# Kernel optimization log

Hardware: AMD Instinct MI355X
Metric: run time of the kernel (lower is better)

## Reference

```python
import jax, jax.numpy as jnp
import numpy as np

V = 256      # vocab_size (hard-coded in source)
H = 2048     # hidden_size
S = 2048     # encoder input length
T = 2048     # decoder target length


def _gru_cell(x, h, w_ih, w_hh, b_ih, b_hh):
    # PyTorch GRU cell math. x, h: [H]; w_ih, w_hh: [3H, H]; b_*: [3H]
    gi = w_ih @ x + b_ih
    gh = w_hh @ h + b_hh
    i_r, i_z, i_n = jnp.split(gi, 3)
    h_r, h_z, h_n = jnp.split(gh, 3)
    r = jax.nn.sigmoid(i_r + h_r)
    z = jax.nn.sigmoid(i_z + h_z)
    n = jnp.tanh(i_n + r * h_n)
    return (1.0 - z) * n + z * h


def setup_inputs() -> dict:
    key = jax.random.key(0)
    ks = jax.random.split(key, 16)
    k = 1.0 / np.sqrt(H)
    u = lambda kk, shape: jax.random.uniform(kk, shape, jnp.float32, -k, k)
    return {
        "inputs": jax.random.randint(ks[0], (S,), 0, V),
        "targets": jax.random.randint(ks[1], (T,), 0, V),
        "emb": jax.random.normal(ks[2], (V, H), jnp.float32),
        "enc_w_ih": u(ks[3], (3 * H, H)),
        "enc_w_hh": u(ks[4], (3 * H, H)),
        "enc_b_ih": u(ks[5], (3 * H,)),
        "enc_b_hh": u(ks[6], (3 * H,)),
        "dec_w_ih": u(ks[7], (3 * H, H)),
        "dec_w_hh": u(ks[8], (3 * H, H)),
        "dec_b_ih": u(ks[9], (3 * H,)),
        "dec_b_hh": u(ks[10], (3 * H,)),
        "fc_w": u(ks[11], (V, H)),
        "fc_b": u(ks[12], (V,)),
    }


def reference(inputs, targets, emb, enc_w_ih, enc_w_hh, enc_b_ih, enc_b_hh,
              dec_w_ih, dec_w_hh, dec_b_ih, dec_b_hh, fc_w, fc_b):
    # Encoder: run GRU over embedded input sequence, keep final state.
    enc_x = emb[inputs]                      # [S, H]
    h0 = jnp.zeros((H,), dtype=emb.dtype)

    def enc_step(h, x):
        return _gru_cell(x, h, enc_w_ih, enc_w_hh, enc_b_ih, enc_b_hh), None

    h_enc, _ = jax.lax.scan(enc_step, h0, enc_x)

    # Decoder token stream: step 0 uses token 0; every later step uses the
    # SAME token targets[1] (faithful to the bug in the original source).
    dec_tokens = jnp.where(jnp.arange(T) == 0, 0, targets[1])  # [T]
    dec_x = emb[dec_tokens]                  # [T, H]

    def dec_step(h, x):
        h_new = _gru_cell(x, h, dec_w_ih, dec_w_hh, dec_b_ih, dec_b_hh)
        return h_new, h_new

    _, dec_hs = jax.lax.scan(dec_step, h_enc, dec_x)  # [T, H]

    # Output projection (batch dim of 1 squeezed away as in the original).
    return dec_hs @ fc_w.T + fc_b            # [T, V]
```

## Files before the change

### kernel.cpp

```cpp
#include <hip/hip_runtime.h>
#include <hip/hip_fp16.h>

#define Hh 2048
#define VV 256
#define SS 2048
#define TT 2048
#define NB 128
#define NT 512

typedef _Float16 h4 __attribute__((ext_vector_type(4)));
typedef _Float16 h2 __attribute__((ext_vector_type(2)));
typedef unsigned int u32x4 __attribute__((ext_vector_type(4)));
typedef unsigned short u16x4 __attribute__((ext_vector_type(4)));

#if defined(__has_builtin)
#if __has_builtin(__builtin_amdgcn_fdot2)
#define FDOT2(a, b, c) __builtin_amdgcn_fdot2((a), (b), (c), false)
#endif
#endif
#ifndef FDOT2
#define FDOT2(a, b, c) \
  fmaf((float)(a).x, (float)(b).x, fmaf((float)(a).y, (float)(b).y, (c)))
#endif

#define SH(v, a, b) __builtin_shufflevector((v), (v), (a), (b))

__global__ __launch_bounds__(256) void gemm_nt(const float* __restrict__ A,
                                               const float* __restrict__ B,
                                               const float* __restrict__ biasM,
                                               const float* __restrict__ biasN,
                                               float* __restrict__ C,
                                               int M, int N, int K) {
  __shared__ __align__(16) float At[32][68];
  __shared__ __align__(16) float Bt[32][68];
  const int t = threadIdx.x;
  const int m0 = blockIdx.x << 6, n0 = blockIdx.y << 6;
  const int r0 = t >> 3, c4 = (t & 7) << 2;
  const int tm = (t >> 4) << 2, tn = (t & 15) << 2;
  float acc[4][4];
#pragma unroll
  for (int i = 0; i < 4; ++i)
#pragma unroll
    for (int j = 0; j < 4; ++j) acc[i][j] = 0.f;

  for (int k0 = 0; k0 < K; k0 += 32) {
    float4 a0 = *(const float4*)&A[(size_t)(m0 + r0) * K + k0 + c4];
    float4 a1 = *(const float4*)&A[(size_t)(m0 + r0 + 32) * K + k0 + c4];
    float4 b0 = *(const float4*)&B[(size_t)(n0 + r0) * K + k0 + c4];
    float4 b1 = *(const float4*)&B[(size_t)(n0 + r0 + 32) * K + k0 + c4];
    __syncthreads();
    At[c4 + 0][r0] = a0.x; At[c4 + 1][r0] = a0.y; At[c4 + 2][r0] = a0.z; At[c4 + 3][r0] = a0.w;
    At[c4 + 0][r0 + 32] = a1.x; At[c4 + 1][r0 + 32] = a1.y; At[c4 + 2][r0 + 32] = a1.z; At[c4 + 3][r0 + 32] = a1.w;
    Bt[c4 + 0][r0] = b0.x; Bt[c4 + 1][r0] = b0.y; Bt[c4 + 2][r0] = b0.z; Bt[c4 + 3][r0] = b0.w;
    Bt[c4 + 0][r0 + 32] = b1.x; Bt[c4 + 1][r0 + 32] = b1.y; Bt[c4 + 2][r0 + 32] = b1.z; Bt[c4 + 3][r0 + 32] = b1.w;
    __syncthreads();
#pragma unroll
    for (int k = 0; k < 32; ++k) {
      float4 av = *(const float4*)&At[k][tm];
      float4 bv = *(const float4*)&Bt[k][tn];
      acc[0][0] = fmaf(av.x, bv.x, acc[0][0]);
      acc[0][1] = fmaf(av.x, bv.y, acc[0][1]);
      acc[0][2] = fmaf(av.x, bv.z, acc[0][2]);
      acc[0][3] = fmaf(av.x, bv.w, acc[0][3]);
      acc[1][0] = fmaf(av.y, bv.x, acc[1][0]);
      acc[1][1] = fmaf(av.y, bv.y, acc[1][1]);
      acc[1][2] = fmaf(av.y, bv.z, acc[1][2]);
      acc[1][3] = fmaf(av.y, bv.w, acc[1][3]);
      acc[2][0] = fmaf(av.z, bv.x, acc[2][0]);
      acc[2][1] = fmaf(av.z, bv.y, acc[2][1]);
      acc[2][2] = fmaf(av.z, bv.z, acc[2][2]);
      acc[2][3] = fmaf(av.z, bv.w, acc[2][3]);
      acc[3][0] = fmaf(av.w, bv.x, acc[3][0]);
      acc[3][1] = fmaf(av.w, bv.y, acc[3][1]);
      acc[3][2] = fmaf(av.w, bv.z, acc[3][2]);
      acc[3][3] = fmaf(av.w, bv.w, acc[3][3]);
    }
  }
#pragma unroll
  for (int i = 0; i < 4; ++i) {
    float bm = biasM ? biasM[m0 + tm + i] : 0.f;
#pragma unroll
    for (int j = 0; j < 4; ++j) {
      float bn = biasN ? biasN[n0 + tn + j] : 0.f;
      C[(size_t)(m0 + tm + i) * N + n0 + tn + j] = acc[i][j] + bm + bn;
    }
  }
}

__global__ __launch_bounds__(NT) void recur_kernel(
    const float* __restrict__ giT_enc, const float* __restrict__ giT_dec,
    const float* __restrict__ enc_w_hh, const float* __restrict__ enc_b_hh,
    const float* __restrict__ dec_w_hh, const float* __restrict__ dec_b_hh,
    const int* __restrict__ inputs, const int* __restrict__ targets,
    unsigned int* __restrict__ hb, float* __restrict__ dec_hs) {
  __shared__ __align__(16) float gi_lds[48 * VV];
  __shared__ __align__(16) _Float16 h16[2][Hh];
  __shared__ __align__(16) unsigned short tok_lds[SS];
  __shared__ float gidec_lds[96];

  const int t = threadIdx.x;
  const int b = blockIdx.x;
  const int bks = b << 4;
  const int w = t >> 6, l = t & 63;
  const int ri = (w << 1) + (l & 1);

  h4 wregA[24], wregB[24];
  float br_, bz_, bn_;
  auto load_wb = [&](const float* W, const float* B) {
#pragma unroll
    for (int g = 0; g < 3; ++g) {
      const float* r0 = W + ((size_t)(g * Hh + bks + (w << 1) + 0)) * Hh + (l << 2);
      const float* r1 = W + ((size_t)(g * Hh + bks + (w << 1) + 1)) * Hh + (l << 2);
#pragma unroll
      for (int q = 0; q < 8; ++q) {
        float4 v0 = *(const float4*)&r0[q * 256];
        float4 v1 = *(const float4*)&r1[q * 256];
        wregA[g * 8 + q] = h4{(_Float16)v0.x, (_Float16)v0.y,
                             (_Float16)v0.z, (_Float16)v0.w};
        wregB[g * 8 + q] = h4{(_Float16)v1.x, (_Float16)v1.y,
                             (_Float16)v1.z, (_Float16)v1.w};
      }
    }
    br_ = B[bks + ri];
    bz_ = B[Hh + bks + ri];
    bn_ = B[2 * Hh + bks + ri];
  };
  load_wb(enc_w_hh, enc_b_hh);

  for (int r = 0; r < 48; ++r) {
    const int g = r >> 4, rr = r & 15;
    const float4* src = (const float4*)(giT_enc + ((size_t)(g * Hh + bks + rr)) * VV);
    if (t < 64) ((float4*)&gi_lds[r * VV])[t] = src[t];
  }

  for (int u = t; u < SS; u += NT) tok_lds[u] = (unsigned short)inputs[u];

  if (t < 96) {
    const int sel = t / 48, r48 = t % 48;
    const int tk = sel ? targets[1] : 0;
    const int g = r48 >> 4, rr = r48 & 15;
    gidec_lds[sel * 48 + r48] = giT_dec[((size_t)(g * Hh + bks + rr)) * VV + tk];
  }

  if (t < 16) {
    __hip_atomic_store(&hb[bks + t], 0x00010000u, __ATOMIC_RELAXED,
                       __HIP_MEMORY_SCOPE_AGENT);
  }
  float hprev = 0.0f;

  for (int step = 0; step < SS + TT; ++step) {
    if (step == SS) load_wb(dec_w_hh, dec_b_hh);
    const int sb = step & 1;

    {
      const unsigned int* addr = hb + ((size_t)sb << 11) + (t << 2);
      const unsigned int want = ((unsigned int)(step + 1)) << 16;
      u32x4 v;
      for (;;) {
        asm volatile(
            "global_load_dwordx4 %0, %1, off sc0 sc1\n\t"
            "s_waitcnt vmcnt(0)"
            : "=&v"(v)
            : "v"(addr)
            : "memory");
        if ((v.x & 0xFFFF0000u) == want && (v.y & 0xFFFF0000u) == want &&
            (v.z & 0xFFFF0000u) == want && (v.w & 0xFFFF0000u) == want)
          break;
        __builtin_amdgcn_s_sleep(1);
      }
      u16x4 hu = {(unsigned short)v.x, (unsigned short)v.y,
                  (unsigned short)v.z, (unsigned short)v.w};
      *(u16x4*)&h16[sb][t << 2] = hu;
    }
    __syncthreads();

    float arA = 0.f, azA = 0.f, anA = 0.f;
    float arB = 0.f, azB = 0.f, anB = 0.f;
#pragma unroll
    for (int q = 0; q < 8; ++q) {
      const int c = q * 256 + (l << 2);
      h4 hv = *(const h4*)&h16[sb][c];
      h2 hlo = SH(hv, 0, 1);
      h2 hhi = SH(hv, 2, 3);
      h4 a_r = wregA[q], a_z = wregA[8 + q], a_n = wregA[16 + q];
      h4 b_r = wregB[q], b_z = wregB[8 + q], b_n = wregB[16 + q];
      arA = FDOT2(SH(a_r, 0, 1), hlo, arA); arA = FDOT2(SH(a_r, 2, 3), hhi, arA);
      azA = FDOT2(SH(a_z, 0, 1), hlo, azA); azA = FDOT2(SH(a_z, 2, 3), hhi, azA);
      anA = FDOT2(SH(a_n, 0, 1), hlo, anA); anA = FDOT2(SH(a_n, 2, 3), hhi, anA);
      arB = FDOT2(SH(b_r, 0, 1), hlo, arB); arB = FDOT2(SH(b_r, 2, 3), hhi, arB);
      azB = FDOT2(SH(b_z, 0, 1), hlo, azB); azB = FDOT2(SH(b_z, 2, 3), hhi, azB);
      anB = FDOT2(SH(b_n, 0, 1), hlo, anB); anB = FDOT2(SH(b_n, 2, 3), hhi, anB);
    }

    float gr, gz, gn;
    if (step < SS) {
      const int tk = tok_lds[step];
      gr = gi_lds[(0 + ri) * VV + tk];
      gz = gi_lds[(16 + ri) * VV + tk];
      gn = gi_lds[(32 + ri) * VV + tk];
    } else {
      const int sel = (step == SS) ? 0 : 48;
      gr = gidec_lds[sel + 0 + ri];
      gz = gidec_lds[sel + 16 + ri];
      gn = gidec_lds[sel + 32 + ri];
    }

#pragma unroll
    for (int off = 32; off > 0; off >>= 1) {
      arA += __shfl_xor(arA, off); azA += __shfl_xor(azA, off); anA += __shfl_xor(anA, off);
      arB += __shfl_xor(arB, off); azB += __shfl_xor(azB, off); anB += __shfl_xor(anB, off);
    }

    if (l < 2) {
      const float ar = l ? arB : arA;
      const float az = l ? azB : azA;
      const float an = l ? anB : anA;
      const float xr = gr + ar + br_;
      const float xz = gz + az + bz_;
      const float hn = an + bn_;
      const float rr = 1.f / (1.f + __expf(-xr));
      const float zz = 1.f / (1.f + __expf(-xz));
      const float nn = tanhf(gn + rr * hn);
      const float hnew = (1.f - zz) * nn + zz * hprev;

      _Float16 hf = (_Float16)hnew;
      const unsigned int pk =
          (((unsigned int)(step + 2)) << 16) |
          (unsigned int)__builtin_bit_cast(unsigned short, hf);
      __hip_atomic_store(&hb[(((size_t)((step + 1) & 1)) << 11) + bks + ri], pk,
                         __ATOMIC_RELAXED, __HIP_MEMORY_SCOPE_AGENT);
      if (step >= SS) dec_hs[(size_t)(step - SS) * Hh + bks + ri] = hnew;
      hprev = hnew;
    }
  }
}

extern "C" void kernel_launch(void* const* d_in, const int* in_sizes, int n_in,
                              void* d_out, int out_size, void* d_ws, size_t ws_size,
                              hipStream_t stream) {
  (void)in_sizes; (void)n_in; (void)out_size; (void)ws_size;
  const int* inputs = (const int*)d_in[0];
  const int* targets = (const int*)d_in[1];
  const float* emb = (const float*)d_in[2];
  const float* enc_w_ih = (const float*)d_in[3];
  const float* enc_w_hh = (const float*)d_in[4];
  const float* enc_b_ih = (const float*)d_in[5];
  const float* enc_b_hh = (const float*)d_in[6];
  const float* dec_w_ih = (const float*)d_in[7];
  const float* dec_w_hh = (const float*)d_in[8];
  const float* dec_b_ih = (const float*)d_in[9];
  const float* dec_b_hh = (const float*)d_in[10];
  const float* fc_w = (const float*)d_in[11];
  const float* fc_b = (const float*)d_in[12];
  float* out = (float*)d_out;

  float* giT_enc = (float*)d_ws;
  float* giT_dec = giT_enc + (size_t)6144 * 256;
  float* dec_hs = giT_dec + (size_t)6144 * 256;
  unsigned int* hb =
      (unsigned int*)(dec_hs + (size_t)TT * Hh);

  gemm_nt<<<dim3(96, 4), 256, 0, stream>>>(enc_w_ih, emb, enc_b_ih, nullptr,
                                           giT_enc, 3 * Hh, VV, Hh);
  gemm_nt<<<dim3(96, 4), 256, 0, stream>>>(dec_w_ih, emb, dec_b_ih, nullptr,
                                           giT_dec, 3 * Hh, VV, Hh);

  void* args[] = {&giT_enc, &giT_dec, &enc_w_hh, &enc_b_hh, &dec_w_hh,
                  &dec_b_hh, &inputs, &targets, &hb, &dec_hs};
  hipError_t e = hipLaunchCooperativeKernel((void*)recur_kernel, dim3(NB),
                                            dim3(NT), args, 0, stream);
  if (e != hipSuccess) {
    recur_kernel<<<dim3(NB), dim3(NT), 0, stream>>>(
        giT_enc, giT_dec, enc_w_hh, enc_b_hh, dec_w_hh, dec_b_hh, inputs,
        targets, hb, dec_hs);
  }

  gemm_nt<<<dim3(32, 4), 256, 0, stream>>>(dec_hs, fc_w, nullptr, fc_b, out,
                                           TT, VV, Hh);
}
```

Measured before the change: 14.90 ms.

## Halve persistent recurrence blocks, each handling 32 hidden rows with 4 rows per wave

The persistent GRU recurrence kernel now runs on 64 blocks instead of 128. Each block owns 32 hidden units and each wave computes 4 rows, so it holds twice as many fp16 weights in registers and twice the gi table in LDS. The aim is to cut the number of blocks that poll the global h buffer each step, which lowers inter-block synchronization cost. In exchange, per-step compute per wave doubles, register pressure roughly doubles (96 h4 weight registers), and LDS use grows, which could cause spills.

Result: slower. 17.37 ms (+16.5%).

```diff
diff --git a/kernel.cpp b/kernel.cpp
--- a/kernel.cpp
+++ b/kernel.cpp
@@ -5,7 +5,7 @@
 #define VV 256
 #define SS 2048
 #define TT 2048
-#define NB 128
+#define NB 64
 #define NT 512
 
 typedef _Float16 h4 __attribute__((ext_vector_type(4)));
@@ -93,32 +93,32 @@
     const float* __restrict__ dec_w_hh, const float* __restrict__ dec_b_hh,
     const int* __restrict__ inputs, const int* __restrict__ targets,
     unsigned int* __restrict__ hb, float* __restrict__ dec_hs) {
-  __shared__ __align__(16) float gi_lds[48 * VV];
+  __shared__ __align__(16) float gi_lds[96 * VV];
   __shared__ __align__(16) _Float16 h16[2][Hh];
   __shared__ __align__(16) unsigned short tok_lds[SS];
-  __shared__ float gidec_lds[96];
+  __shared__ float gidec_lds[192];
 
   const int t = threadIdx.x;
   const int b = blockIdx.x;
-  const int bks = b << 4;
+  const int bks = b << 5;
   const int w = t >> 6, l = t & 63;
-  const int ri = (w << 1) + (l & 1);
-
-  h4 wregA[24], wregB[24];
+  const int ri = (w << 2) + (l & 3);
+
+  h4 wreg[4][24];
   float br_, bz_, bn_;
   auto load_wb = [&](const float* W, const float* B) {
 #pragma unroll
-    for (int g = 0; g < 3; ++g) {
-      const float* r0 = W + ((size_t)(g * Hh + bks + (w << 1) + 0)) * Hh + (l << 2);
-      const float* r1 = W + ((size_t)(g * Hh + bks + (w << 1) + 1)) * Hh + (l << 2);
-#pragma unroll
-      for (int q = 0; q < 8; ++q) {
-        float4 v0 = *(const float4*)&r0[q * 256];
-        float4 v1 = *(const float4*)&r1[q * 256];
-        wregA[g * 8 + q] = h4{(_Float16)v0.x, (_Float16)v0.y,
-                             (_Float16)v0.z, (_Float16)v0.w};
-        wregB[g * 8 + q] = h4{(_Float16)v1.x, (_Float16)v1.y,
-                             (_Float16)v1.z, (_Float16)v1.w};
+    for (int r = 0; r < 4; ++r) {
+#pragma unroll
+      for (int g = 0; g < 3; ++g) {
+        const float* rb =
+            W + ((size_t)(g * Hh + bks + (w << 2) + r)) * Hh + (l << 2);
+#pragma unroll
+        for (int q = 0; q < 8; ++q) {
+          float4 vv = *(const float4*)&rb[q * 256];
+          wreg[r][g * 8 + q] = h4{(_Float16)vv.x, (_Float16)vv.y,
+                                  (_Float16)vv.z, (_Float16)vv.w};
+        }
       }
     }
     br_ = B[bks + ri];
@@ -127,22 +127,23 @@
   };
   load_wb(enc_w_hh, enc_b_hh);
 
-  for (int r = 0; r < 48; ++r) {
-    const int g = r >> 4, rr = r & 15;
-    const float4* src = (const float4*)(giT_enc + ((size_t)(g * Hh + bks + rr)) * VV);
-    if (t < 64) ((float4*)&gi_lds[r * VV])[t] = src[t];
+  for (int i = t; i < 96 * 64; i += NT) {
+    const int r = i >> 6, c = i & 63;
+    const int g = r >> 5, rr = r & 31;
+    ((float4*)&gi_lds[r * VV])[c] =
+        ((const float4*)(giT_enc + ((size_t)(g * Hh + bks + rr)) * VV))[c];
   }
 
   for (int u = t; u < SS; u += NT) tok_lds[u] = (unsigned short)inputs[u];
 
-  if (t < 96) {
-    const int sel = t / 48, r48 = t % 48;
+  if (t < 192) {
+    const int sel = t / 96, r96 = t % 96;
     const int tk = sel ? targets[1] : 0;
-    const int g = r48 >> 4, rr = r48 & 15;
-    gidec_lds[sel * 48 + r48] = giT_dec[((size_t)(g * Hh + bks + rr)) * VV + tk];
-  }
-
-  if (t < 16) {
+    const int g = r96 >> 5, rr = r96 & 31;
+    gidec_lds[sel * 96 + r96] = giT_dec[((size_t)(g * Hh + bks + rr)) * VV + tk];
+  }
+
+  if (t < 32) {
     __hip_atomic_store(&hb[bks + t], 0x00010000u, __ATOMIC_RELAXED,
                        __HIP_MEMORY_SCOPE_AGENT);
   }
@@ -174,50 +175,60 @@
     }
     __syncthreads();
 
-    float arA = 0.f, azA = 0.f, anA = 0.f;
-    float arB = 0.f, azB = 0.f, anB = 0.f;
+    float ar[4], az[4], an[4];
+#pragma unroll
+    for (int r = 0; r < 4; ++r) { ar[r] = 0.f; az[r] = 0.f; an[r] = 0.f; }
 #pragma unroll
     for (int q = 0; q < 8; ++q) {
       const int c = q * 256 + (l << 2);
       h4 hv = *(const h4*)&h16[sb][c];
       h2 hlo = SH(hv, 0, 1);
       h2 hhi = SH(hv, 2, 3);
-      h4 a_r = wregA[q], a_z = wregA[8 + q], a_n = wregA[16 + q];
-      h4 b_r = wregB[q], b_z = wregB[8 + q], b_n = wregB[16 + q];
-      arA = FDOT2(SH(a_r, 0, 1), hlo, arA); arA = FDOT2(SH(a_r, 2, 3), hhi, arA);
-      azA = FDOT2(SH(a_z, 0, 1), hlo, azA); azA = FDOT2(SH(a_z, 2, 3), hhi, azA);
-      anA = FDOT2(SH(a_n, 0, 1), hlo, anA); anA = FDOT2(SH(a_n, 2, 3), hhi, anA);
-      arB = FDOT2(SH(b_r, 0, 1), hlo, arB); arB = FDOT2(SH(b_r, 2, 3), hhi, arB);
-      azB = FDOT2(SH(b_z, 0, 1), hlo, azB); azB = FDOT2(SH(b_z, 2, 3), hhi, azB);
-      anB = FDOT2(SH(b_n, 0, 1), hlo, anB); anB = FDOT2(SH(b_n, 2, 3), hhi, anB);
+#pragma unroll
+      for (int r = 0; r < 4; ++r) {
+        h4 wr4 = wreg[r][q], wz4 = wreg[r][8 + q], wn4 = wreg[r][16 + q];
+        ar[r] = FDOT2(SH(wr4, 0, 1), hlo, ar[r]);
+        ar[r] = FDOT2(SH(wr4, 2, 3), hhi, ar[r]);
+        az[r] = FDOT2(SH(wz4, 0, 1), hlo, az[r]);
+        az[r] = FDOT2(SH(wz4, 2, 3), hhi, az[r]);
+        an[r] = FDOT2(SH(wn4, 0, 1), hlo, an[r]);
+        an[r] = FDOT2(SH(wn4, 2, 3), hhi, an[r]);
+      }
     }
 
     float gr, gz, gn;
     if (step < SS) {
       const int tk = tok_lds[step];
       gr = gi_lds[(0 + ri) * VV + tk];
-      gz = gi_lds[(16 + ri) * VV + tk];
-      gn = gi_lds[(32 + ri) * VV + tk];
+      gz = gi_lds[(32 + ri) * VV + tk];
+      gn = gi_lds[(64 + ri) * VV + tk];
     } else {
-      const int sel = (step == SS) ? 0 : 48;
+      const int sel = (step == SS) ? 0 : 96;
       gr = gidec_lds[sel + 0 + ri];
-      gz = gidec_lds[sel + 16 + ri];
-      gn = gidec_lds[sel + 32 + ri];
+      gz = gidec_lds[sel + 32 + ri];
+      gn = gidec_lds[sel + 64 + ri];
     }
 
 #pragma unroll
     for (int off = 32; off > 0; off >>= 1) {
-      arA += __shfl_xor(arA, off); azA += __shfl_xor(azA, off); anA += __shfl_xor(anA, off);
-      arB += __shfl_xor(arB, off); azB += __shfl_xor(azB, off); anB += __shfl_xor(anB, off);
-    }
-
-    if (l < 2) {
-      const float ar = l ? arB : arA;
-      const float az = l ? azB : azA;
-      const float an = l ? anB : anA;
-      const float xr = gr + ar + br_;
-      const float xz = gz + az + bz_;
-      const float hn = an + bn_;
+#pragma unroll
+      for (int r = 0; r < 4; ++r) {
+        ar[r] += __shfl_xor(ar[r], off);
+        az[r] += __shfl_xor(az[r], off);
+        an[r] += __shfl_xor(an[r], off);
+      }
+    }
+
+    if (l < 4) {
+      const float arS = (l & 2) ? ((l & 1) ? ar[3] : ar[2])
+                                : ((l & 1) ? ar[1] : ar[0]);
+      const float azS = (l & 2) ? ((l & 1) ? az[3] : az[2])
+                                : ((l & 1) ? az[1] : az[0]);
+      const float anS = (l & 2) ? ((l & 1) ? an[3] : an[2])
+                                : ((l & 1) ? an[1] : an[0]);
+      const float xr = gr + arS + br_;
+      const float xz = gz + azS + bz_;
+      const float hn = anS + bn_;
       const float rr = 1.f / (1.f + __expf(-xr));
       const float zz = 1.f / (1.f + __expf(-xz));
       const float nn = tanhf(gn + rr * hn);
```
